# Kernel tuning notes

Measured on AMD Instinct MI355X. Metric: run time of the kernel, lower is better.

Reference implementation:

```python
import jax, jax.numpy as jnp
import numpy as np

T = 120  # hard-coded timestep count in the original forward


def gru_scan(x, W_ih, W_hh, b_ih, b_hh):
    """Run a torch-style GRUCell over time. x: [B, T, D] -> outputs [B, T, H]."""
    B = x.shape[0]
    H = W_hh.shape[1]

    def step(h, xt):
        gi = xt @ W_ih.T + b_ih          # [B, 3H]
        gh = h @ W_hh.T + b_hh           # [B, 3H]
        i_r, i_z, i_n = jnp.split(gi, 3, axis=-1)
        h_r, h_z, h_n = jnp.split(gh, 3, axis=-1)
        r = jax.nn.sigmoid(i_r + h_r)
        z = jax.nn.sigmoid(i_z + h_z)
        n = jnp.tanh(i_n + r * h_n)
        h_new = (1.0 - z) * n + z * h
        return h_new, h_new

    h0 = jnp.zeros((B, H), x.dtype)
    _, ys = jax.lax.scan(step, h0, jnp.swapaxes(x, 0, 1))  # ys: [T, B, H]
    return jnp.swapaxes(ys, 0, 1)


def setup_inputs() -> dict:
    key = jax.random.key(0)
    ks = jax.random.split(key, 20)
    B, Dc, Da, H, A = 2048, 128, 96, 256, 40
    s = 0.05
    inp = {
        "crime_input": jax.random.normal(ks[0], (B, T, Dc), jnp.float32),
        "anomaly_input": jax.random.normal(ks[1], (B, T, Da), jnp.float32),
        # gru_crime
        "W_ih_c": jax.random.normal(ks[2], (3 * H, Dc), jnp.float32) * s,
        "W_hh_c": jax.random.normal(ks[3], (3 * H, H), jnp.float32) * s,
        "b_ih_c": jax.random.normal(ks[4], (3 * H,), jnp.float32) * s,
        "b_hh_c": jax.random.normal(ks[5], (3 * H,), jnp.float32) * s,
        # gru_anomaly
        "W_ih_a": jax.random.normal(ks[6], (3 * H, Da), jnp.float32) * s,
        "W_hh_a": jax.random.normal(ks[7], (3 * H, H), jnp.float32) * s,
        "b_ih_a": jax.random.normal(ks[8], (3 * H,), jnp.float32) * s,
        "b_hh_a": jax.random.normal(ks[9], (3 * H,), jnp.float32) * s,
        # gru_inter (input = 2H)
        "W_ih_i": jax.random.normal(ks[10], (3 * H, 2 * H), jnp.float32) * s,
        "W_hh_i": jax.random.normal(ks[11], (3 * H, H), jnp.float32) * s,
        "b_ih_i": jax.random.normal(ks[12], (3 * H,), jnp.float32) * s,
        "b_hh_i": jax.random.normal(ks[13], (3 * H,), jnp.float32) * s,
        # attention
        "Wv": jax.random.normal(ks[14], (A, H), jnp.float32) * s,
        "bv": jax.random.normal(ks[15], (A,), jnp.float32) * s,
        "wu": jax.random.normal(ks[16], (A,), jnp.float32) * s,
    }
    return inp


def reference(crime_input, anomaly_input,
              W_ih_c, W_hh_c, b_ih_c, b_hh_c,
              W_ih_a, W_hh_a, b_ih_a, b_hh_a,
              W_ih_i, W_hh_i, b_ih_i, b_hh_i,
              Wv, bv, wu):
    # dropout layers are identity in eval mode
    out_c = gru_scan(crime_input, W_ih_c, W_hh_c, b_ih_c, b_hh_c)      # [B,T,H]
    out_a = gru_scan(anomaly_input, W_ih_a, W_hh_a, b_ih_a, b_hh_a)    # [B,T,H]
    inp_i = jnp.concatenate([out_c, out_a], axis=2)                    # [B,T,2H]
    out_i = gru_scan(inp_i, W_ih_i, W_hh_i, b_ih_i, b_hh_i)            # [B,T,H]

    um = jnp.tanh(jnp.einsum('bth,ah->bta', out_i, Wv) + bv)           # [B,T,A]
    scores = jnp.einsum('bta,a->bt', um, wu)                           # [B,T]
    alpha = jax.nn.softmax(scores, axis=1)                             # [B,T]
    context = jnp.einsum('bt,bth->bh', alpha, out_i)[:, None, :]       # [B,1,H]
    return context
```

## Files before the change

### kernel.cpp

```cpp
#include <hip/hip_runtime.h>

typedef float  f32x4  __attribute__((ext_vector_type(4)));
typedef short  short8 __attribute__((ext_vector_type(8)));
typedef __bf16 bf16x8 __attribute__((ext_vector_type(8)));

#define B_SZ 2048
#define T_SZ 120
#define H_SZ 256
#define G3   768
#define A_SZ 40

#define MFMA_BF16 __builtin_amdgcn_mfma_f32_16x16x32_bf16

union U8 { short8 s; bf16x8 b; };
__device__ __forceinline__ bf16x8 as_bf(short8 s){ U8 u; u.s = s; return u.b; }

__device__ __forceinline__ unsigned short f2bf(float x){
  unsigned u = __float_as_uint(x);
  return (unsigned short)((u + 0x7FFFu + ((u >> 16) & 1u)) >> 16);
}
__device__ __forceinline__ float bf2f(unsigned short h){
  return __uint_as_float(((unsigned)h) << 16);
}
__device__ __forceinline__ void cvt_hilo(float x, short& hi, short& lo){
  unsigned short h = f2bf(x);
  hi = (short)h;
  lo = (short)f2bf(x - bf2f(h));
}
__device__ __forceinline__ float sigm(float x){ return 1.0f / (1.0f + __expf(-x)); }
__device__ __forceinline__ float tanh_(float x){
  float a = fabsf(x);
  float t = 1.0f - 2.0f / (__expf(2.0f * a) + 1.0f);
  return copysignf(t, x);
}

__global__ void zinit(float* __restrict__ p, size_t n){
  size_t i = (size_t)blockIdx.x * 256 + threadIdx.x;
  size_t stride = (size_t)gridDim.x * 256;
  for (; i < n; i += stride) p[i] = 0.0f;
}

__global__ void packall(const float* __restrict__ WihC, const float* __restrict__ WhhC,
                        const float* __restrict__ WihA, const float* __restrict__ WhhA,
                        const float* __restrict__ WihI, const float* __restrict__ WhhI,
                        const float* __restrict__ Wv,
                        short* __restrict__ pIhC, short* __restrict__ pHhC,
                        short* __restrict__ pIhA, short* __restrict__ pHhA,
                        short* __restrict__ pIhI, short* __restrict__ pHhI,
                        short* __restrict__ pWvT)
{
  int b = blockIdx.x;
  int lane = threadIdx.x;
  const float* src; short* dst; int K;
  if      (b < 192)  { src = WihC; dst = pIhC; K = 128; }
  else if (b < 576)  { b -= 192;  src = WhhC; dst = pHhC; K = 256; }
  else if (b < 720)  { b -= 576;  src = WihA; dst = pIhA; K = 96;  }
  else if (b < 1104) { b -= 720;  src = WhhA; dst = pHhA; K = 256; }
  else if (b < 1872) { b -= 1104; src = WihI; dst = pIhI; K = 512; }
  else if (b < 2256) { b -= 1872; src = WhhI; dst = pHhI; K = 256; }
  else {
    int bb = b - 2256;
    int q = bb >> 3, kt = bb & 7;
    int a = q * 16 + (lane & 15);
    int k = kt * 32 + (lane >> 4) * 8;
    size_t o = (((size_t)q * 8 + kt) * 64 + lane) * 8;
#pragma unroll
    for (int i = 0; i < 8; i++){
      float v = (a < A_SZ) ? Wv[(size_t)a * H_SZ + k + i] : 0.0f;
      pWvT[o + i] = (short)f2bf(v);
    }
    return;
  }
  int KT = K >> 5;
  int nt = b / KT, kt = b % KT;
  const float* s = src + (size_t)(nt * 16 + (lane & 15)) * K + kt * 32 + (lane >> 4) * 8;
  size_t o = (((size_t)nt * KT + kt) * 64 + lane) * 8;
#pragma unroll
  for (int i = 0; i < 8; i++) dst[o + i] = (short)f2bf(s[i]);
}

__device__ __forceinline__ void gemm_body(
    int bid, const short* __restrict__ A, const short* __restrict__ Bhi,
    const float* __restrict__ b1, const float* __restrict__ b2,
    float* __restrict__ C, short* Ash)
{
  int tid = threadIdx.x;
  int w = tid >> 6, lane = tid & 63;
  int mg = w & 1, ng = w >> 1;
  int m0 = bid * 64;
  int nb = ng * 12;
  const int KT = 16;

  {
    int r = tid >> 3, s0 = (tid & 7) * 64;
    const short* src = A + (size_t)(m0 + r) * 512 + s0;
    short* dst = Ash + r * 520 + s0;
#pragma unroll
    for (int i = 0; i < 8; i++)
      *(short8*)(dst + i * 8) = *(const short8*)(src + i * 8);
  }
  __syncthreads();

  const f32x4 zero = {0.f, 0.f, 0.f, 0.f};
  f32x4 acc[2][12];
#pragma unroll
  for (int f = 0; f < 2; f++)
#pragma unroll
    for (int q = 0; q < 12; q++) acc[f][q] = zero;

  int rr = lane & 15, ks = lane >> 4;
  const short* Ap[2];
#pragma unroll
  for (int f = 0; f < 2; f++)
    Ap[f] = Ash + (mg * 32 + f * 16 + rr) * 520 + ks * 8;

  for (int kt = 0; kt < KT; ++kt){
    bf16x8 ahb[2];
#pragma unroll
    for (int f = 0; f < 2; f++)
      ahb[f] = as_bf(*(const short8*)(Ap[f] + kt * 32));
#pragma unroll
    for (int q = 0; q < 12; q++){
      int bo = (((nb + q) * KT + kt) * 64 + lane) * 8;
      bf16x8 bh = as_bf(*(const short8*)(Bhi + bo));
#pragma unroll
      for (int f = 0; f < 2; f++)
        acc[f][q] = MFMA_BF16(ahb[f], bh, acc[f][q], 0, 0, 0);
    }
  }
  int nc = lane & 15;
  int rb = lane >> 4;
#pragma unroll
  for (int q = 0; q < 12; q++){
    int n = (nb + q) * 16 + nc;
    float bias = b1[n] + (n < 512 ? b2[n] : 0.0f);
#pragma unroll
    for (int f = 0; f < 2; f++)
#pragma unroll
      for (int i = 0; i < 4; i++)
        C[(size_t)(m0 + mg * 32 + f * 16 + rb * 4 + i) * G3 + n] = acc[f][q][i] + bias;
  }
}

template<int D, int KI>
__device__ __forceinline__ void leaf_body(
    const float* __restrict__ x, const short* __restrict__ Wih,
    const short* __restrict__ Whh, const float* __restrict__ bih,
    const float* __restrict__ bhh, short* __restrict__ outp, int ooff,
    float* __restrict__ hs, int b0, int t0, int tcnt,
    short* hhi, short* hlo, short* xhi)
{
  constexpr int XP  = D + 8;
  constexpr int NST = 2 * D;
  constexpr int CPR = D / 8;
  int tid = threadIdx.x, w = tid >> 6, lane = tid & 63;
  int arow = lane & 15, kgrp = lane >> 4;
  int c0 = w * 16 + arow;
  int msk = (arow & 7) << 4;

  float bir[2], biz[2], bin_[2], bhn[2];
#pragma unroll
  for (int j = 0; j < 2; j++){
    int c = c0 + j * 128;
    bir[j] = bih[c] + bhh[c];
    biz[j] = bih[256 + c] + bhh[256 + c];
    bin_[j] = bih[512 + c];
    bhn[j] = bhh[512 + c];
  }

  int srow = tid / CPR, scol = (tid % CPR) * 8;
  bool stg = tid < NST;
  const float* sx = x + ((size_t)(b0 + srow) * T_SZ + t0) * D + scol;
  short* xwh = xhi + srow * XP + scol;

  int orow = tid >> 5, oc8 = (tid & 31) * 8;
  const char* ordp = (const char*)hhi + orow * 512 + ((oc8 * 2) ^ ((orow & 7) << 4));
  short* owp = outp + (size_t)(b0 + orow) * tcnt * 512 + ooff + oc8;

  float hreg[2][4];
#pragma unroll
  for (int j = 0; j < 2; j++)
#pragma unroll
  for (int i = 0; i < 4; i++){
    int row = kgrp * 4 + i, c = c0 + j * 128;
    float v = hs[(size_t)(b0 + row) * H_SZ + c];
    hreg[j][i] = v;
    short h_, l_; cvt_hilo(v, h_, l_);
    int off = row * 512 + ((c * 2) ^ ((row & 7) << 4));
    *(short*)((char*)hhi + off) = h_;
    *(short*)((char*)hlo + off) = l_;
  }
  if (stg){
    f32x4 a0 = *(const f32x4*)sx;
    f32x4 a1 = *(const f32x4*)(sx + 4);
    short8 h8;
#pragma unroll
    for (int i = 0; i < 4; i++){ h8[i] = (short)f2bf(a0[i]); h8[4+i] = (short)f2bf(a1[i]); }
    *(short8*)xwh = h8;
  }
  __syncthreads();

  const char* hhp = (const char*)hhi + arow * 512;
  const char* hlp = (const char*)hlo + arow * 512;
  const char* xhp = (const char*)xhi + (arow * XP + kgrp * 8) * 2;

  const f32x4 zero = {0.f, 0.f, 0.f, 0.f};
  for (int t = 0; t < tcnt; t++){
    if (t > 0)
      *(short8*)(owp + (size_t)(t - 1) * 512) = *(const short8*)ordp;

    f32x4 acc[6], accNi[2];
#pragma unroll
    for (int q = 0; q < 6; q++) acc[q] = zero;
    accNi[0] = zero; accNi[1] = zero;

    short8 wb[6], wn[6];
#pragma unroll
    for (int q = 0; q < 6; q++)
      wb[q] = *(const short8*)(Wih + (((w + 8 * q) * KI) * 64 + lane) * 8);
#pragma unroll
    for (int kt = 0; kt < KI; kt++){
      if (kt + 1 < KI){
#pragma unroll
        for (int q = 0; q < 6; q++)
          wn[q] = *(const short8*)(Wih + (((w + 8 * q) * KI + kt + 1) * 64 + lane) * 8);
      }
      bf16x8 ah = as_bf(*(const short8*)(xhp + kt * 64));
#pragma unroll
      for (int q = 0; q < 6; q++){
        bf16x8 bw = as_bf(wb[q]);
        if (q < 4) acc[q] = MFMA_BF16(ah, bw, acc[q], 0, 0, 0);
        else       accNi[q-4] = MFMA_BF16(ah, bw, accNi[q-4], 0, 0, 0);
      }
      if (kt + 1 < KI){
#pragma unroll
        for (int q = 0; q < 6; q++) wb[q] = wn[q];
      }
    }
#pragma unroll
    for (int q = 0; q < 6; q++)
      wb[q] = *(const short8*)(Whh + (((w + 8 * q) * 8) * 64 + lane) * 8);
#pragma unroll
    for (int kt = 0; kt < 8; kt++){
      if (kt < 7){
#pragma unroll
        for (int q = 0; q < 6; q++)
          wn[q] = *(const short8*)(Whh + (((w + 8 * q) * 8 + kt + 1) * 64 + lane) * 8);
      }
      int kb = (kt * 64 + kgrp * 16) ^ msk;
      bf16x8 ah = as_bf(*(const short8*)(hhp + kb));
      bf16x8 al = as_bf(*(const short8*)(hlp + kb));
#pragma unroll
      for (int q = 0; q < 6; q++){
        bf16x8 bw = as_bf(wb[q]);
        acc[q] = MFMA_BF16(ah, bw, acc[q], 0, 0, 0);
        acc[q] = MFMA_BF16(al, bw, acc[q], 0, 0, 0);
      }
      if (kt < 7){
#pragma unroll
        for (int q = 0; q < 6; q++) wb[q] = wn[q];
      }
    }
    __syncthreads();

    f32x4 a0, a1;
    bool ds = stg && (t + 1 < tcnt);
    if (ds){
      a0 = *(const f32x4*)(sx + (size_t)(t + 1) * D);
      a1 = *(const f32x4*)(sx + (size_t)(t + 1) * D + 4);
    }

#pragma unroll
    for (int j = 0; j < 2; j++)
#pragma unroll
    for (int i = 0; i < 4; i++){
      float rr = sigm(acc[j][i] + bir[j]);
      float zz = sigm(acc[2 + j][i] + biz[j]);
      float nn = tanh_(accNi[j][i] + bin_[j] + rr * (acc[4 + j][i] + bhn[j]));
      float hv = (1.0f - zz) * nn + zz * hreg[j][i];
      hreg[j][i] = hv;
      int row = kgrp * 4 + i, c = c0 + j * 128;
      short h_, l_; cvt_hilo(hv, h_, l_);
      int off = row * 512 + ((c * 2) ^ ((row & 7) << 4));
      *(short*)((char*)hhi + off) = h_;
      *(short*)((char*)hlo + off) = l_;
    }
    if (ds){
      short8 h8;
#pragma unroll
      for (int i = 0; i < 4; i++){ h8[i] = (short)f2bf(a0[i]); h8[4+i] = (short)f2bf(a1[i]); }
      *(short8*)xwh = h8;
    }
    __syncthreads();
  }

  *(short8*)(owp + (size_t)(tcnt - 1) * 512) = *(const short8*)ordp;

#pragma unroll
  for (int j = 0; j < 2; j++)
#pragma unroll
  for (int i = 0; i < 4; i++){
    int row = kgrp * 4 + i;
    hs[(size_t)(b0 + row) * H_SZ + c0 + j * 128] = hreg[j][i];
  }
}

__device__ __forceinline__ void inter_body(
    int bid, const float* __restrict__ gi,
    const short* __restrict__ Whh, const float* __restrict__ bhh,
    const short* __restrict__ WvT,
    const float* __restrict__ bv, const float* __restrict__ wu,
    float* __restrict__ ctx, float* __restrict__ lsum,
    float* __restrict__ hs, int tcnt,
    short* hhi, short* hlo, short* wvl, float* esh)
{
  int b0 = bid * 16;
  int tid = threadIdx.x, w = tid >> 6, lane = tid & 63;
  int arow = lane & 15, kgrp = lane >> 4;
  int c0 = w * 16 + arow;
  int msk = (arow & 7) << 4;

  float bhn[2];
  bhn[0] = bhh[512 + c0];
  bhn[1] = bhh[512 + c0 + 128];

  float wuv[3], bvv[3];
#pragma unroll
  for (int q = 0; q < 3; q++){
    int a = q * 16 + arow;
    wuv[q] = (a < A_SZ) ? wu[a] : 0.0f;
    bvv[q] = (a < A_SZ) ? bv[a] : 0.0f;
  }

  for (int i = tid; i < 3 * 8 * 64; i += 512)
    *(short8*)(wvl + i * 8) = *(const short8*)(WvT + (size_t)i * 8);

  float hreg[2][4];
#pragma unroll
  for (int j = 0; j < 2; j++)
#pragma unroll
  for (int i = 0; i < 4; i++){
    int row = kgrp * 4 + i, c = c0 + j * 128;
    float v = hs[(size_t)(b0 + row) * H_SZ + c];
    hreg[j][i] = v;
    short h_, l_; cvt_hilo(v, h_, l_);
    int off = row * 512 + ((c * 2) ^ ((row & 7) << 4));
    *(short*)((char*)hhi + off) = h_;
    *(short*)((char*)hlo + off) = l_;
  }
  __syncthreads();

  const char* hhp = (const char*)hhi + arow * 512;
  const char* hlp = (const char*)hlo + arow * 512;
  const float* gp[4];
#pragma unroll
  for (int i = 0; i < 4; i++)
    gp[i] = gi + (size_t)(b0 + kgrp * 4 + i) * tcnt * G3;

  float ctxa[2][4] = {{0.f,0.f,0.f,0.f},{0.f,0.f,0.f,0.f}};
  float lsr[4] = {0.f, 0.f, 0.f, 0.f};

  const f32x4 zero = {0.f, 0.f, 0.f, 0.f};
  for (int t = 0; t < tcnt; t++){
    float gvr[2][4], gvz[2][4], gvn[2][4];
#pragma unroll
    for (int j = 0; j < 2; j++)
#pragma unroll
    for (int i = 0; i < 4; i++){
      const float* g = gp[i] + (size_t)t * G3 + c0 + j * 128;
      gvr[j][i] = g[0];
      gvz[j][i] = g[256];
      gvn[j][i] = g[512];
    }

    f32x4 acc[6];
#pragma unroll
    for (int q = 0; q < 6; q++) acc[q] = zero;

    short8 wb[6], wn[6];
#pragma unroll
    for (int q = 0; q < 6; q++)
      wb[q] = *(const short8*)(Whh + (((w + 8 * q) * 8) * 64 + lane) * 8);
#pragma unroll
    for (int kt = 0; kt < 8; kt++){
      if (kt < 7){
#pragma unroll
        for (int q = 0; q < 6; q++)
          wn[q] = *(const short8*)(Whh + (((w + 8 * q) * 8 + kt + 1) * 64 + lane) * 8);
      }
      int kb = (kt * 64 + kgrp * 16) ^ msk;
      bf16x8 ah = as_bf(*(const short8*)(hhp + kb));
      bf16x8 al = as_bf(*(const short8*)(hlp + kb));
#pragma unroll
      for (int q = 0; q < 6; q++){
        bf16x8 bw = as_bf(wb[q]);
        acc[q] = MFMA_BF16(ah, bw, acc[q], 0, 0, 0);
        acc[q] = MFMA_BF16(al, bw, acc[q], 0, 0, 0);
      }
      if (kt < 7){
#pragma unroll
        for (int q = 0; q < 6; q++) wb[q] = wn[q];
      }
    }

    if (w == 0 && t > 0){
      f32x4 um[3];
#pragma unroll
      for (int q = 0; q < 3; q++) um[q] = zero;
#pragma unroll
      for (int kt = 0; kt < 8; kt++){
        int kb = (kt * 64 + kgrp * 16) ^ msk;
        bf16x8 ah = as_bf(*(const short8*)(hhp + kb));
#pragma unroll
        for (int q = 0; q < 3; q++){
          bf16x8 bw = as_bf(*(const short8*)(wvl + ((q * 8 + kt) * 64 + lane) * 8));
          um[q] = MFMA_BF16(ah, bw, um[q], 0, 0, 0);
        }
      }
      f32x4 sp;
#pragma unroll
      for (int i = 0; i < 4; i++){
        float v = 0.f;
#pragma unroll
        for (int q = 0; q < 3; q++)
          v += wuv[q] * tanh_(um[q][i] + bvv[q]);
        sp[i] = v;
      }
#pragma unroll
      for (int d = 1; d < 16; d <<= 1){
#pragma unroll
        for (int i = 0; i < 4; i++)
          sp[i] += __shfl_xor(sp[i], d);
      }
      if (arow == 0){
#pragma unroll
        for (int i = 0; i < 4; i++){
          float e = __expf(sp[i]);
          esh[kgrp * 4 + i] = e;
          lsr[i] += e;
        }
      }
    }
    __syncthreads();

    if (t > 0){
#pragma unroll
      for (int i = 0; i < 4; i++){
        float e = esh[kgrp * 4 + i];
#pragma unroll
        for (int j = 0; j < 2; j++)
          ctxa[j][i] += e * hreg[j][i];
      }
    }

#pragma unroll
    for (int j = 0; j < 2; j++)
#pragma unroll
    for (int i = 0; i < 4; i++){
      float rr = sigm(gvr[j][i] + acc[j][i]);
      float zz = sigm(gvz[j][i] + acc[2 + j][i]);
      float nn = tanh_(gvn[j][i] + rr * (acc[4 + j][i] + bhn[j]));
      float hv = (1.0f - zz) * nn + zz * hreg[j][i];
      hreg[j][i] = hv;
      int row = kgrp * 4 + i, c = c0 + j * 128;
      short h_, l_; cvt_hilo(hv, h_, l_);
      int off = row * 512 + ((c * 2) ^ ((row & 7) << 4));
      *(short*)((char*)hhi + off) = h_;
      *(short*)((char*)hlo + off) = l_;
    }
    __syncthreads();
  }

  if (w == 0){
    f32x4 um[3];
#pragma unroll
    for (int q = 0; q < 3; q++) um[q] = zero;
#pragma unroll
    for (int kt = 0; kt < 8; kt++){
      int kb = (kt * 64 + kgrp * 16) ^ msk;
      bf16x8 ah = as_bf(*(const short8*)(hhp + kb));
#pragma unroll
      for (int q = 0; q < 3; q++){
        bf16x8 bw = as_bf(*(const short8*)(wvl + ((q * 8 + kt) * 64 + lane) * 8));
        um[q] = MFMA_BF16(ah, bw, um[q], 0, 0, 0);
      }
    }
    f32x4 sp;
#pragma unroll
    for (int i = 0; i < 4; i++){
      float v = 0.f;
#pragma unroll
      for (int q = 0; q < 3; q++)
        v += wuv[q] * tanh_(um[q][i] + bvv[q]);
      sp[i] = v;
    }
#pragma unroll
    for (int d = 1; d < 16; d <<= 1){
#pragma unroll
      for (int i = 0; i < 4; i++)
        sp[i] += __shfl_xor(sp[i], d);
    }
    if (arow == 0){
#pragma unroll
      for (int i = 0; i < 4; i++){
        float e = __expf(sp[i]);
        esh[kgrp * 4 + i] = e;
        lsr[i] += e;
      }
    }
  }
  __syncthreads();
#pragma unroll
  for (int i = 0; i < 4; i++){
    float e = esh[kgrp * 4 + i];
#pragma unroll
    for (int j = 0; j < 2; j++)
      ctxa[j][i] += e * hreg[j][i];
  }

#pragma unroll
  for (int j = 0; j < 2; j++)
#pragma unroll
  for (int i = 0; i < 4; i++){
    int row = kgrp * 4 + i;
    hs[(size_t)(b0 + row) * H_SZ + c0 + j * 128] = hreg[j][i];
    ctx[(size_t)(b0 + row) * H_SZ + c0 + j * 128] += ctxa[j][i];
  }
  if (w == 0 && arow == 0){
#pragma unroll
    for (int i = 0; i < 4; i++)
      lsum[b0 + kgrp * 4 + i] += lsr[i];
  }
}

__global__ __launch_bounds__(512, 2) void fused3(
    int nIb, int nLb,
    const float* __restrict__ giI, const short* __restrict__ WhhI_,
    const float* __restrict__ bhhI_, const short* __restrict__ WvT,
    const float* __restrict__ bv, const float* __restrict__ wu,
    float* __restrict__ ctx, float* __restrict__ lsum,
    float* __restrict__ hsI, int tcntI,
    const float* __restrict__ x0, const short* __restrict__ WihL0,
    const short* __restrict__ WhhL0, const float* __restrict__ bihL0,
    const float* __restrict__ bhhL0,
    const float* __restrict__ x1, const short* __restrict__ WihL1,
    const short* __restrict__ WhhL1, const float* __restrict__ bihL1,
    const float* __restrict__ bhhL1,
    short* __restrict__ outL, float* __restrict__ hsC, float* __restrict__ hsA,
    int t0L, int tcntL,
    const short* __restrict__ Ag, const short* __restrict__ BhiG,
    const float* __restrict__ b1G, const float* __restrict__ b2G,
    float* __restrict__ Cg)
{
  __shared__ short smem[64 * 520];
  int bid = blockIdx.x;
  if (bid < nIb){
    inter_body(bid, giI, WhhI_, bhhI_, WvT, bv, wu, ctx, lsum, hsI, tcntI,
               smem, smem + 4096, smem + 8192, (float*)(smem + 20480));
  } else if (bid < nIb + nLb){
    int lb = bid - nIb;
    short* hhi = smem;
    short* hlo = smem + 4096;
    short* xhi = smem + 8192;
    if (lb < 128)
      leaf_body<128, 4>(x0, WihL0, WhhL0, bihL0, bhhL0, outL, 0, hsC,
                        lb * 16, t0L, tcntL, hhi, hlo, xhi);
    else
      leaf_body<96, 3>(x1, WihL1, WhhL1, bihL1, bhhL1, outL, 256, hsA,
                       (lb - 128) * 16, t0L, tcntL, hhi, hlo, xhi);
  } else {
    gemm_body(bid - nIb - nLb, Ag, BhiG, b1G, b2G, Cg, smem);
  }
}

__global__ __launch_bounds__(256, 1) void attn_fin(
    const float* __restrict__ ctx, const float* __restrict__ lsum,
    float* __restrict__ out)
{
  int b = blockIdx.x, tid = threadIdx.x;
  out[(size_t)b * H_SZ + tid] = ctx[(size_t)b * H_SZ + tid] / lsum[b];
}

extern "C" void kernel_launch(void* const* d_in, const int* in_sizes, int n_in,
                              void* d_out, int out_size, void* d_ws, size_t ws_size,
                              hipStream_t stream)
{
  (void)in_sizes; (void)n_in; (void)out_size;
  const float* crime = (const float*)d_in[0];
  const float* anom  = (const float*)d_in[1];
  const float* WihC = (const float*)d_in[2];
  const float* WhhC = (const float*)d_in[3];
  const float* bihC = (const float*)d_in[4];
  const float* bhhC = (const float*)d_in[5];
  const float* WihA = (const float*)d_in[6];
  const float* WhhA = (const float*)d_in[7];
  const float* bihA = (const float*)d_in[8];
  const float* bhhA = (const float*)d_in[9];
  const float* WihI = (const float*)d_in[10];
  const float* WhhI = (const float*)d_in[11];
  const float* bihI = (const float*)d_in[12];
  const float* bhhI = (const float*)d_in[13];
  const float* Wv = (const float*)d_in[14];
  const float* bv = (const float*)d_in[15];
  const float* wu = (const float*)d_in[16];
  float* out = (float*)d_out;

  char* ws = (char*)d_ws;
  size_t off = 0;
  auto take = [&](size_t n){ size_t r = off; off += (n + 255) & ~(size_t)255; return r; };

  short* pIhC = (short*)(ws + take((size_t)G3 * 128 * 2));
  short* pHhC = (short*)(ws + take((size_t)G3 * 256 * 2));
  short* pIhA = (short*)(ws + take((size_t)G3 * 96 * 2));
  short* pHhA = (short*)(ws + take((size_t)G3 * 256 * 2));
  short* pIhI = (short*)(ws + take((size_t)G3 * 512 * 2));
  short* pHhI = (short*)(ws + take((size_t)G3 * 256 * 2));
  short* pWvT = (short*)(ws + take((size_t)3 * 8 * 64 * 8 * 2));

  size_t state_off = off;
  float* hsC  = (float*)(ws + take((size_t)B_SZ * H_SZ * 4));
  float* hsA  = (float*)(ws + take((size_t)B_SZ * H_SZ * 4));
  float* hsI  = (float*)(ws + take((size_t)B_SZ * H_SZ * 4));
  float* ctx  = (float*)(ws + take((size_t)B_SZ * H_SZ * 4));
  float* lsum = (float*)(ws + take((size_t)B_SZ * 4));
  size_t state_end = off;

  size_t per2 = (size_t)B_SZ * (G3 * 4 + 512 * 2) * 2;
  size_t avail = (ws_size > off + 8192) ? (ws_size - off - 8192) : 0;
  int TC = (int)(avail / per2);
  if (TC > 20) TC = 20;
  if (TC < 1) TC = 1;
  if (TC > T_SZ) TC = T_SZ;
  int nc = (T_SZ + TC - 1) / TC;

  float* Gi[2];  short* OcaH[2];
  Gi[0]   = (float*)(ws + take((size_t)B_SZ * TC * G3 * 4));
  Gi[1]   = (float*)(ws + take((size_t)B_SZ * TC * G3 * 4));
  OcaH[0] = (short*)(ws + take((size_t)B_SZ * TC * 512 * 2));
  OcaH[1] = (short*)(ws + take((size_t)B_SZ * TC * 512 * 2));

  auto tcn = [&](int j){
    if (j < 0 || j >= nc) return 0;
    int r = T_SZ - j * TC;
    return r < TC ? r : TC;
  };

  zinit<<<2048, 256, 0, stream>>>((float*)(ws + state_off), (state_end - state_off) / 4);
  packall<<<2280, 64, 0, stream>>>(WihC, WhhC, WihA, WhhA, WihI, WhhI, Wv,
                                   pIhC, pHhC, pIhA, pHhA, pIhI, pHhI, pWvT);

  for (int k = 0; k <= nc + 1; k++){
    int tL = tcn(k), tG = tcn(k - 1), tI = tcn(k - 2);
    int nLb = tL ? 256 : 0;
    int nGb = tG ? (B_SZ * tG) / 64 : 0;
    int nIb = tI ? 128 : 0;
    int grid = nIb + nLb + nGb;
    if (grid == 0) continue;
    fused3<<<grid, 512, 0, stream>>>(
        nIb, nLb,
        Gi[k & 1], pHhI, bhhI, pWvT, bv, wu, ctx, lsum, hsI, tI,
        crime, pIhC, pHhC, bihC, bhhC,
        anom,  pIhA, pHhA, bihA, bhhA,
        OcaH[k & 1], hsC, hsA, k * TC, tL,
        OcaH[(k - 1) & 1], pIhI, bihI, bhhI, Gi[(k - 1) & 1]);
  }
  attn_fin<<<B_SZ, 256, 0, stream>>>(ctx, lsum, out);
}
```

Measured before the change: 3.160 ms.

## Process 32 batch rows per leaf GRU block to reuse weight fragments

The leaf GRU blocks now handle 32 batch rows instead of 16, so each weight fragment loaded from global memory feeds two MFMAs (one per 16-row half). The leaf block count drops from 256 to 128, which halves total weight traffic per timestep. In exchange, the explicit register double-buffering of weights is removed, accumulator and hidden-state registers double, shared-memory offsets grow, and fewer blocks are available for parallelism alongside the concurrent GEMM and inter blocks.

```diff
diff --git a/kernel.cpp b/kernel.cpp
--- a/kernel.cpp
+++ b/kernel.cpp
@@ -143,7 +143,7 @@
 }
 
 template<int D, int KI>
-__device__ __forceinline__ void leaf_body(
+__device__ __forceinline__ void leaf32_body(
     const float* __restrict__ x, const short* __restrict__ Wih,
     const short* __restrict__ Whh, const float* __restrict__ bih,
     const float* __restrict__ bhh, short* __restrict__ outp, int ooff,
@@ -151,7 +151,7 @@
     short* hhi, short* hlo, short* xhi)
 {
   constexpr int XP  = D + 8;
-  constexpr int NST = 2 * D;
+  constexpr int NST = 4 * D;
   constexpr int CPR = D / 8;
   int tid = threadIdx.x, w = tid >> 6, lane = tid & 63;
   int arow = lane & 15, kgrp = lane >> 4;
@@ -173,18 +173,21 @@
   const float* sx = x + ((size_t)(b0 + srow) * T_SZ + t0) * D + scol;
   short* xwh = xhi + srow * XP + scol;
 
-  int orow = tid >> 5, oc8 = (tid & 31) * 8;
-  const char* ordp = (const char*)hhi + orow * 512 + ((oc8 * 2) ^ ((orow & 7) << 4));
-  short* owp = outp + (size_t)(b0 + orow) * tcnt * 512 + ooff + oc8;
-
-  float hreg[2][4];
+  int orow = tid >> 4, ocb = (tid & 15) * 16;
+  const char* ord0 = (const char*)hhi + orow * 512 + ((ocb * 2) ^ ((orow & 7) << 4));
+  const char* ord1 = (const char*)hhi + orow * 512 + (((ocb + 8) * 2) ^ ((orow & 7) << 4));
+  short* owp = outp + (size_t)(b0 + orow) * tcnt * 512 + ooff + ocb;
+
+  float hreg[2][2][4];
+#pragma unroll
+  for (int f = 0; f < 2; f++)
 #pragma unroll
   for (int j = 0; j < 2; j++)
 #pragma unroll
   for (int i = 0; i < 4; i++){
-    int row = kgrp * 4 + i, c = c0 + j * 128;
+    int row = f * 16 + kgrp * 4 + i, c = c0 + j * 128;
     float v = hs[(size_t)(b0 + row) * H_SZ + c];
-    hreg[j][i] = v;
+    hreg[f][j][i] = v;
     short h_, l_; cvt_hilo(v, h_, l_);
     int off = row * 512 + ((c * 2) ^ ((row & 7) << 4));
     *(short*)((char*)hhi + off) = h_;
@@ -200,65 +203,70 @@
   }
   __syncthreads();
 
-  const char* hhp = (const char*)hhi + arow * 512;
-  const char* hlp = (const char*)hlo + arow * 512;
-  const char* xhp = (const char*)xhi + (arow * XP + kgrp * 8) * 2;
+  const char *hhp[2], *hlp[2], *xhp[2];
+#pragma unroll
+  for (int f = 0; f < 2; f++){
+    hhp[f] = (const char*)hhi + (f * 16 + arow) * 512;
+    hlp[f] = (const char*)hlo + (f * 16 + arow) * 512;
+    xhp[f] = (const char*)xhi + ((f * 16 + arow) * XP + kgrp * 8) * 2;
+  }
 
   const f32x4 zero = {0.f, 0.f, 0.f, 0.f};
   for (int t = 0; t < tcnt; t++){
-    if (t > 0)
-      *(short8*)(owp + (size_t)(t - 1) * 512) = *(const short8*)ordp;
-
-    f32x4 acc[6], accNi[2];
-#pragma unroll
-    for (int q = 0; q < 6; q++) acc[q] = zero;
-    accNi[0] = zero; accNi[1] = zero;
-
-    short8 wb[6], wn[6];
-#pragma unroll
-    for (int q = 0; q < 6; q++)
-      wb[q] = *(const short8*)(Wih + (((w + 8 * q) * KI) * 64 + lane) * 8);
+    if (t > 0){
+      *(short8*)(owp + (size_t)(t - 1) * 512) = *(const short8*)ord0;
+      *(short8*)(owp + (size_t)(t - 1) * 512 + 8) = *(const short8*)ord1;
+    }
+
+    f32x4 acc[2][6], accNi[2][2];
+#pragma unroll
+    for (int f = 0; f < 2; f++){
+#pragma unroll
+      for (int q = 0; q < 6; q++) acc[f][q] = zero;
+      accNi[f][0] = zero; accNi[f][1] = zero;
+    }
+
 #pragma unroll
     for (int kt = 0; kt < KI; kt++){
-      if (kt + 1 < KI){
-#pragma unroll
-        for (int q = 0; q < 6; q++)
-          wn[q] = *(const short8*)(Wih + (((w + 8 * q) * KI + kt + 1) * 64 + lane) * 8);
-      }
-      bf16x8 ah = as_bf(*(const short8*)(xhp + kt * 64));
+      short8 wb[6];
+#pragma unroll
+      for (int q = 0; q < 6; q++)
+        wb[q] = *(const short8*)(Wih + (((w + 8 * q) * KI + kt) * 64 + lane) * 8);
+      bf16x8 ah[2];
+#pragma unroll
+      for (int f = 0; f < 2; f++)
+        ah[f] = as_bf(*(const short8*)(xhp[f] + kt * 64));
 #pragma unroll
       for (int q = 0; q < 6; q++){
         bf16x8 bw = as_bf(wb[q]);
-        if (q < 4) acc[q] = MFMA_BF16(ah, bw, acc[q], 0, 0, 0);
-        else       accNi[q-4] = MFMA_BF16(ah, bw, accNi[q-4], 0, 0, 0);
-      }
-      if (kt + 1 < KI){
-#pragma unroll
-        for (int q = 0; q < 6; q++) wb[q] = wn[q];
-      }
-    }
-#pragma unroll
-    for (int q = 0; q < 6; q++)
-      wb[q] = *(const short8*)(Whh + (((w + 8 * q) * 8) * 64 + lane) * 8);
+#pragma unroll
+        for (int f = 0; f < 2; f++){
+          if (q < 4) acc[f][q] = MFMA_BF16(ah[f], bw, acc[f][q], 0, 0, 0);
+          else       accNi[f][q-4] = MFMA_BF16(ah[f], bw, accNi[f][q-4], 0, 0, 0);
+        }
+      }
+    }
 #pragma unroll
     for (int kt = 0; kt < 8; kt++){
-      if (kt < 7){
-#pragma unroll
-        for (int q = 0; q < 6; q++)
-          wn[q] = *(const short8*)(Whh + (((w + 8 * q) * 8 + kt + 1) * 64 + lane) * 8);
-      }
+      short8 wb[6];
+#pragma unroll
+      for (int q = 0; q < 6; q++)
+        wb[q] = *(const short8*)(Whh + (((w + 8 * q) * 8 + kt) * 64 + lane) * 8);
       int kb = (kt * 64 + kgrp * 16) ^ msk;
-      bf16x8 ah = as_bf(*(const short8*)(hhp + kb));
-      bf16x8 al = as_bf(*(const short8*)(hlp + kb));
+      bf16x8 ah[2], al[2];
+#pragma unroll
+      for (int f = 0; f < 2; f++){
+        ah[f] = as_bf(*(const short8*)(hhp[f] + kb));
+        al[f] = as_bf(*(const short8*)(hlp[f] + kb));
+      }
 #pragma unroll
       for (int q = 0; q < 6; q++){
         bf16x8 bw = as_bf(wb[q]);
-        acc[q] = MFMA_BF16(ah, bw, acc[q], 0, 0, 0);
-        acc[q] = MFMA_BF16(al, bw, acc[q], 0, 0, 0);
-      }
-      if (kt < 7){
-#pragma unroll
-        for (int q = 0; q < 6; q++) wb[q] = wn[q];
+#pragma unroll
+        for (int f = 0; f < 2; f++){
+          acc[f][q] = MFMA_BF16(ah[f], bw, acc[f][q], 0, 0, 0);
+          acc[f][q] = MFMA_BF16(al[f], bw, acc[f][q], 0, 0, 0);
+        }
       }
     }
     __syncthreads();
@@ -271,15 +279,17 @@
     }
 
 #pragma unroll
+    for (int f = 0; f < 2; f++)
+#pragma unroll
     for (int j = 0; j < 2; j++)
 #pragma unroll
     for (int i = 0; i < 4; i++){
-      float rr = sigm(acc[j][i] + bir[j]);
-      float zz = sigm(acc[2 + j][i] + biz[j]);
-      float nn = tanh_(accNi[j][i] + bin_[j] + rr * (acc[4 + j][i] + bhn[j]));
-      float hv = (1.0f - zz) * nn + zz * hreg[j][i];
-      hreg[j][i] = hv;
-      int row = kgrp * 4 + i, c = c0 + j * 128;
+      float rr = sigm(acc[f][j][i] + bir[j]);
+      float zz = sigm(acc[f][2 + j][i] + biz[j]);
+      float nn = tanh_(accNi[f][j][i] + bin_[j] + rr * (acc[f][4 + j][i] + bhn[j]));
+      float hv = (1.0f - zz) * nn + zz * hreg[f][j][i];
+      hreg[f][j][i] = hv;
+      int row = f * 16 + kgrp * 4 + i, c = c0 + j * 128;
       short h_, l_; cvt_hilo(hv, h_, l_);
       int off = row * 512 + ((c * 2) ^ ((row & 7) << 4));
       *(short*)((char*)hhi + off) = h_;
@@ -294,14 +304,17 @@
     __syncthreads();
   }
 
-  *(short8*)(owp + (size_t)(tcnt - 1) * 512) = *(const short8*)ordp;
-
+  *(short8*)(owp + (size_t)(tcnt - 1) * 512) = *(const short8*)ord0;
+  *(short8*)(owp + (size_t)(tcnt - 1) * 512 + 8) = *(const short8*)ord1;
+
+#pragma unroll
+  for (int f = 0; f < 2; f++)
 #pragma unroll
   for (int j = 0; j < 2; j++)
 #pragma unroll
   for (int i = 0; i < 4; i++){
-    int row = kgrp * 4 + i;
-    hs[(size_t)(b0 + row) * H_SZ + c0 + j * 128] = hreg[j][i];
+    int row = f * 16 + kgrp * 4 + i;
+    hs[(size_t)(b0 + row) * H_SZ + c0 + j * 128] = hreg[f][j][i];
   }
 }
 
@@ -560,14 +573,14 @@
   } else if (bid < nIb + nLb){
     int lb = bid - nIb;
     short* hhi = smem;
-    short* hlo = smem + 4096;
-    short* xhi = smem + 8192;
-    if (lb < 128)
-      leaf_body<128, 4>(x0, WihL0, WhhL0, bihL0, bhhL0, outL, 0, hsC,
-                        lb * 16, t0L, tcntL, hhi, hlo, xhi);
+    short* hlo = smem + 8192;
+    short* xhi = smem + 16384;
+    if (lb < 64)
+      leaf32_body<128, 4>(x0, WihL0, WhhL0, bihL0, bhhL0, outL, 0, hsC,
+                          lb * 32, t0L, tcntL, hhi, hlo, xhi);
     else
-      leaf_body<96, 3>(x1, WihL1, WhhL1, bihL1, bhhL1, outL, 256, hsA,
-                       (lb - 128) * 16, t0L, tcntL, hhi, hlo, xhi);
+      leaf32_body<96, 3>(x1, WihL1, WhhL1, bihL1, bhhL1, outL, 256, hsA,
+                         (lb - 64) * 32, t0L, tcntL, hhi, hlo, xhi);
   } else {
     gemm_body(bid - nIb - nLb, Ag, BhiG, b1G, b2G, Cg, smem);
   }
@@ -651,7 +664,7 @@
 
   for (int k = 0; k <= nc + 1; k++){
     int tL = tcn(k), tG = tcn(k - 1), tI = tcn(k - 2);
-    int nLb = tL ? 256 : 0;
+    int nLb = tL ? 128 : 0;
     int nGb = tG ? (B_SZ * tG) / 64 : 0;
     int nIb = tI ? 128 : 0;
     int grid = nIb + nLb + nGb;
```

After: 3.195 ms. No clear change (+1.1%).
